# Optimization experiments

Hardware: AMD Instinct MI355X
Metric: run time of the kernel (lower is better)

Reference implementation:

```python
import jax, jax.numpy as jnp
import numpy as np

B, D, K = 32, 64, 26      # batch, n_objects, per-object feature dim
QST = 256                  # question embedding size
G = [512, 512, 512, 512, 512, 512, 28]  # g_layers (last = n_answers)
IN = 2 * K                 # in_size = concat(x_i, x_j)
AGG = 4                    # aggregation + question injection position


def setup_inputs() -> dict:
    key = jax.random.key(0)
    ks = jax.random.split(key, 2 + 2 * len(G))
    inp = {
        "x": jax.random.normal(ks[0], (B, D, K), jnp.float32),
        "qst": jax.random.normal(ks[1], (B, QST), jnp.float32),
    }
    prev = IN
    for i, g in enumerate(G):
        d_in = prev + (QST if i == AGG else 0)
        inp[f"W{i}"] = jax.random.normal(ks[2 + 2 * i], (g, d_in), jnp.float32) * (1.0 / np.sqrt(d_in))
        inp[f"b{i}"] = jnp.zeros((g,), jnp.float32)
        prev = g
    return inp


def reference(x, qst, W0, b0, W1, b1, W2, b2, W3, b3, W4, b4, W5, b5, W6, b6):
    b, d, k = x.shape
    # all ordered pairs: x_full[b, p, q] = [x[b, q], x[b, p]]  (matches torch repeat/cat order)
    xi = jnp.broadcast_to(x[:, None, :, :], (b, d, d, k))
    xj = jnp.broadcast_to(x[:, :, None, :], (b, d, d, k))
    h = jnp.concatenate([xi, xj], axis=-1).reshape(b * d * d, 2 * k)
    Ws = [W0, W1, W2, W3, W4, W5, W6]
    bs = [b0, b1, b2, b3, b4, b5, b6]
    n = len(Ws)
    for i in range(n):
        if i == AGG:
            # sum-aggregation over all d^2 pairs, then question injection
            h = h.reshape(b, d * d, h.shape[-1]).sum(axis=1)  # [b, g]
            h = jnp.concatenate([h, qst], axis=1)             # [b, g+qst]
        h = h @ Ws[i].T + bs[i]
        if i != n - 1:
            h = jax.nn.relu(h)
    return jax.nn.log_softmax(h, axis=1)
```

## Files before the change

kernel.cpp:

```cpp
#include <hip/hip_runtime.h>
#include <math.h>


typedef __attribute__((ext_vector_type(8))) short bf16x8;
typedef __attribute__((ext_vector_type(4))) float f32x4;
typedef __attribute__((ext_vector_type(4))) unsigned int u32x4;

__device__ __forceinline__ unsigned short f2bf(float f) {
    union { float f; unsigned u; } x; x.f = f;
    unsigned r = x.u + 0x7fffu + ((x.u >> 16) & 1u);
    return (unsigned short)(r >> 16);
}

#define NP_WP   786432
#define NP_W0P  32768
#define NP_W4T  393216
#define NP_W5T  262144
#define NP_S    16384
#define NP_TOTAL (NP_WP + NP_W0P + NP_W4T + NP_W5T + NP_S)
__global__ void k_prep(const float* __restrict__ W1, const float* __restrict__ W2,
                       const float* __restrict__ W3, const float* __restrict__ W0,
                       const float* __restrict__ W4, const float* __restrict__ W5,
                       unsigned short* __restrict__ Wp,
                       unsigned short* __restrict__ W0p,
                       float* __restrict__ W4v,
                       float* __restrict__ W5v,
                       float* __restrict__ S)
{
    int f = blockIdx.x * 256 + threadIdx.x;
    if (f < NP_WP) {
        int l = f >> 18, r = f & 262143;
        int n = r >> 9, k = r & 511;
        const float* W = (l == 0) ? W1 : (l == 1) ? W2 : W3;
        float v = W[r];
        int wv = n >> 6, jj = (n >> 4) & 3, i16 = n & 15;
        int s = k >> 5, q4 = (k >> 3) & 3, j = k & 7;
        int lane = q4 * 16 + i16;
        Wp[(size_t)l * 262144 + ((((wv * 16 + s) * 4 + jj) * 64 + lane) << 3) + j] = f2bf(v);
    } else if (f < NP_WP + NP_W0P) {
        int g = f - NP_WP;
        int n = g >> 6, k = g & 63;
        float v = (k < 52) ? W0[n * 52 + k] : 0.f;
        int wv = n >> 6, jj = (n >> 4) & 3, i16 = n & 15;
        int s = k >> 5, q4 = (k >> 3) & 3, j = k & 7;
        int lane = q4 * 16 + i16;
        W0p[((((wv * 2 + s) * 4 + jj) * 64 + lane) << 3) + j] = f2bf(v);
    } else if (f < NP_WP + NP_W0P + NP_W4T) {
        int g = f - (NP_WP + NP_W0P);
        int o = g / 768, k = g % 768;
        W4v[(size_t)((k >> 2) * 512 + o) * 4 + (k & 3)] = W4[g];
    } else if (f < NP_WP + NP_W0P + NP_W4T + NP_W5T) {
        int g = f - (NP_WP + NP_W0P + NP_W4T);
        int o = g >> 9, k = g & 511;
        W5v[(size_t)((k >> 2) * 512 + o) * 4 + (k & 3)] = W5[g];
    } else if (f < NP_TOTAL) {
        S[f - (NP_WP + NP_W0P + NP_W4T + NP_W5T)] = 0.f;
    }
}

__device__ __forceinline__ void store_h(const f32x4 (&acc)[4][4], const float* __restrict__ bl,
                                        unsigned short* hsm, int wave, int i16, int q4, int lane)
{
    char* base = (char*)hsm;
    #pragma unroll
    for (int j = 0; j < 4; ++j) {
        int col = (wave * 4 + j) * 16 + i16;
        int g = col >> 3;
        int e = g & 7;
        float bb = bl[col];
        #pragma unroll
        for (int mt = 0; mt < 4; ++mt) {
            #pragma unroll
            for (int r = 0; r < 4; ++r) {
                int row = mt * 16 + q4 * 4 + r;
                float v = fmaxf(acc[mt][j][r] + bb, 0.f);
                unsigned hv = f2bf(v);
                unsigned sw = (unsigned)__builtin_amdgcn_update_dpp(0, (int)hv, 0xB1, 0xF, 0xF, true);
                if ((lane & 1) == 0) {
                    int slot = row ^ e;
                    *(unsigned*)(base + g * 1024 + slot * 16 + ((col & 7) << 1)) = hv | (sw << 16);
                }
            }
        }
    }
}

__global__ __launch_bounds__(512, 4) void k_fused(
    const float* __restrict__ x,
    const unsigned short* __restrict__ Wp,
    const unsigned short* __restrict__ W0p,
    const float* __restrict__ b0, const float* __restrict__ b1,
    const float* __restrict__ b2, const float* __restrict__ b3,
    float* __restrict__ S)
{
    __shared__ __align__(16) unsigned short hsm[64 * 512];
    __shared__ __align__(16) unsigned short xs[8 * 64 * 8];
    int t = threadIdx.x;
    int blk = blockIdx.x;
    int b = blk >> 6, p = blk & 63;

    {
        int row = t >> 3, gr = t & 7;
        const float* xq = x + (size_t)(b * 64 + row) * 26;
        const float* xp = x + (size_t)(b * 64 + p) * 26;
        unsigned w[4];
        #pragma unroll
        for (int h = 0; h < 4; ++h) {
            int k0 = gr * 8 + h * 2;
            int k1 = k0 + 1;
            float f0 = (k0 < 26) ? xq[k0] : (k0 < 52 ? xp[k0 - 26] : 0.f);
            float f1 = (k1 < 26) ? xq[k1] : (k1 < 52 ? xp[k1 - 26] : 0.f);
            w[h] = (unsigned)f2bf(f0) | ((unsigned)f2bf(f1) << 16);
        }
        *(u32x4*)((char*)xs + gr * 1024 + ((row ^ gr) << 4)) = (u32x4){w[0], w[1], w[2], w[3]};
    }

    int wave = t >> 6, lane = t & 63;
    int i16 = lane & 15, q4 = lane >> 4;

    f32x4 acc[4][4];

    __syncthreads();

    {
        #pragma unroll
        for (int mt = 0; mt < 4; ++mt)
            #pragma unroll
            for (int j = 0; j < 4; ++j)
                acc[mt][j] = (f32x4){0.f, 0.f, 0.f, 0.f};
        const unsigned short* Bb0 = W0p + wave * 4096 + lane * 8;
        const char* xb = (const char*)xs;
        #pragma unroll
        for (int s = 0; s < 2; ++s) {
            bf16x8 bfr[4];
            #pragma unroll
            for (int j = 0; j < 4; ++j)
                bfr[j] = *(const bf16x8*)(Bb0 + s * 2048 + j * 512);
            int g = s * 4 + q4;
            const char* A0 = xb + g * 1024 + ((i16 ^ g) << 4);
            #pragma unroll
            for (int mt = 0; mt < 4; ++mt) {
                bf16x8 a = *(const bf16x8*)(A0 + mt * 256);
                #pragma unroll
                for (int j = 0; j < 4; ++j)
                    acc[mt][j] = __builtin_amdgcn_mfma_f32_16x16x32_bf16(a, bfr[j], acc[mt][j], 0, 0, 0);
            }
        }
        store_h(acc, b0, hsm, wave, i16, q4, lane);
    }

    int A_even = (q4 << 10) + ((i16 ^ q4) << 4);
    int A_odd  = A_even ^ 64;
    const char* hb = (const char*)hsm;

    #pragma unroll 1
    for (int l = 0; l < 3; ++l) {
        const float* bl = (l == 0) ? b1 : (l == 1) ? b2 : b3;
        __syncthreads();

        #pragma unroll
        for (int mt = 0; mt < 4; ++mt)
            #pragma unroll
            for (int j = 0; j < 4; ++j)
                acc[mt][j] = (f32x4){0.f, 0.f, 0.f, 0.f};

        const unsigned short* Bb = Wp + (size_t)l * 262144 + wave * 32768 + lane * 8;

        #pragma unroll 1
        for (int s = 0; s < 16; ++s) {
            bf16x8 bfr[4];
            #pragma unroll
            for (int j = 0; j < 4; ++j)
                bfr[j] = *(const bf16x8*)(Bb + s * 2048 + j * 512);
            const char* Ab = hb + (s << 12) + ((s & 1) ? A_odd : A_even);
            bf16x8 a0 = *(const bf16x8*)(Ab);
            bf16x8 a1 = *(const bf16x8*)(Ab + 256);
            __builtin_amdgcn_s_setprio(1);
            #pragma unroll
            for (int j = 0; j < 4; ++j)
                acc[0][j] = __builtin_amdgcn_mfma_f32_16x16x32_bf16(a0, bfr[j], acc[0][j], 0, 0, 0);
            #pragma unroll
            for (int j = 0; j < 4; ++j)
                acc[1][j] = __builtin_amdgcn_mfma_f32_16x16x32_bf16(a1, bfr[j], acc[1][j], 0, 0, 0);
            __builtin_amdgcn_s_setprio(0);
            bf16x8 a2 = *(const bf16x8*)(Ab + 512);
            bf16x8 a3 = *(const bf16x8*)(Ab + 768);
            __builtin_amdgcn_s_setprio(1);
            #pragma unroll
            for (int j = 0; j < 4; ++j)
                acc[2][j] = __builtin_amdgcn_mfma_f32_16x16x32_bf16(a2, bfr[j], acc[2][j], 0, 0, 0);
            #pragma unroll
            for (int j = 0; j < 4; ++j)
                acc[3][j] = __builtin_amdgcn_mfma_f32_16x16x32_bf16(a3, bfr[j], acc[3][j], 0, 0, 0);
            __builtin_amdgcn_s_setprio(0);
        }
        __syncthreads();

        if (l < 2) {
            store_h(acc, bl, hsm, wave, i16, q4, lane);
        } else {
            #pragma unroll
            for (int j = 0; j < 4; ++j) {
                int col = (wave * 4 + j) * 16 + i16;
                float bb = bl[col];
                float sum = 0.f;
                #pragma unroll
                for (int mt = 0; mt < 4; ++mt)
                    #pragma unroll
                    for (int r = 0; r < 4; ++r)
                        sum += fmaxf(acc[mt][j][r] + bb, 0.f);
                sum += __shfl_xor(sum, 16);
                sum += __shfl_xor(sum, 32);
                if (q4 == 0) atomicAdd(&S[b * 512 + col], sum);
            }
        }
    }
}

__global__ __launch_bounds__(512) void k_tail(
    const float* __restrict__ S, const float* __restrict__ qst,
    const float* __restrict__ W4v, const float* __restrict__ b4,
    const float* __restrict__ W5v, const float* __restrict__ b5,
    const float* __restrict__ W6, const float* __restrict__ b6,
    float* __restrict__ out)
{
    int b = blockIdx.x, t = threadIdx.x;
    __shared__ __align__(16) float z[768];
    __shared__ __align__(16) float h4[512];
    __shared__ float h5[512];
    __shared__ float logits[28];
    __shared__ float red[2];

    for (int i = t; i < 768; i += 512)
        z[i] = (i < 512) ? S[b * 512 + i] : qst[b * 256 + (i - 512)];
    __syncthreads();
    {
        float acc = b4[t];
        const float4* Wv = (const float4*)W4v;
        const float4* z4 = (const float4*)z;
        #pragma unroll 4
        for (int kb = 0; kb < 192; ++kb) {
            float4 w = Wv[kb * 512 + t];
            float4 zz = z4[kb];
            acc = fmaf(w.x, zz.x, acc);
            acc = fmaf(w.y, zz.y, acc);
            acc = fmaf(w.z, zz.z, acc);
            acc = fmaf(w.w, zz.w, acc);
        }
        h4[t] = fmaxf(acc, 0.f);
    }
    __syncthreads();
    {
        float acc = b5[t];
        const float4* Wv = (const float4*)W5v;
        const float4* h44 = (const float4*)h4;
        #pragma unroll 4
        for (int kb = 0; kb < 128; ++kb) {
            float4 w = Wv[kb * 512 + t];
            float4 hh = h44[kb];
            acc = fmaf(w.x, hh.x, acc);
            acc = fmaf(w.y, hh.y, acc);
            acc = fmaf(w.z, hh.z, acc);
            acc = fmaf(w.w, hh.w, acc);
        }
        h5[t] = fmaxf(acc, 0.f);
    }
    __syncthreads();
    {
        int o = t >> 4, c = t & 15;
        if (o < 28) {
            float acc = 0.f;
            for (int k = c; k < 512; k += 16) acc = fmaf(W6[o * 512 + k], h5[k], acc);
            acc += __shfl_xor(acc, 1);
            acc += __shfl_xor(acc, 2);
            acc += __shfl_xor(acc, 4);
            acc += __shfl_xor(acc, 8);
            if (c == 0) logits[o] = acc + b6[o];
        }
    }
    __syncthreads();
    if (t == 0) {
        float mx = -1e30f;
        for (int cc = 0; cc < 28; ++cc) mx = fmaxf(mx, logits[cc]);
        float se = 0.f;
        for (int cc = 0; cc < 28; ++cc) se += expf(logits[cc] - mx);
        red[0] = mx; red[1] = logf(se);
    }
    __syncthreads();
    if (t < 28) out[b * 28 + t] = logits[t] - red[0] - red[1];
}

extern "C" void kernel_launch(void* const* d_in, const int* in_sizes, int n_in,
                              void* d_out, int out_size, void* d_ws, size_t ws_size,
                              hipStream_t stream)
{
    const float* x   = (const float*)d_in[0];
    const float* qst = (const float*)d_in[1];
    const float* W0  = (const float*)d_in[2];
    const float* b0  = (const float*)d_in[3];
    const float* W1  = (const float*)d_in[4];
    const float* b1  = (const float*)d_in[5];
    const float* W2  = (const float*)d_in[6];
    const float* b2  = (const float*)d_in[7];
    const float* W3  = (const float*)d_in[8];
    const float* b3  = (const float*)d_in[9];
    const float* W4  = (const float*)d_in[10];
    const float* b4  = (const float*)d_in[11];
    const float* W5  = (const float*)d_in[12];
    const float* b5  = (const float*)d_in[13];
    const float* W6  = (const float*)d_in[14];
    const float* b6  = (const float*)d_in[15];
    float* out = (float*)d_out;

    char* ws = (char*)d_ws;
    unsigned short* Wp  = (unsigned short*)(ws);
    unsigned short* W0p = (unsigned short*)(ws + 1572864);
    float*          W4v = (float*)(ws + 1638400);
    float*          W5v = (float*)(ws + 3211264);
    float*          S   = (float*)(ws + 4259840);

    k_prep <<<NP_TOTAL / 256, 256, 0, stream>>>(W1, W2, W3, W0, W4, W5,
                                                Wp, W0p, W4v, W5v, S);
    k_fused<<<2048, 512, 0, stream>>>(x, Wp, W0p, b0, b1, b2, b3, S);
    k_tail <<<32, 512, 0, stream>>>(S, qst, W4v, b4, W5v, b5, W6, b6, out);
}
```

Measured before the change: 370.3 us.

## Double-buffer weight fragments, replace atomics with partial buffer, widen tail kernel

The inner GEMM loop is unrolled by two and prefetches the next k-step's B fragments from global memory while the current step's MFMAs run, hiding load latency. The atomic accumulation into S is replaced by per-block partial sums written to a buffer and reduced in the tail kernel. That also removes the zero-init of S from the prep kernel. The tail kernel now uses 1024 threads and splits the K dimension of layers 4 and 5 into two halves, at the cost of extra registers in the fused kernel and a 4 MB partial buffer read in the tail.

```diff
diff --git a/kernel.cpp b/kernel.cpp
--- a/kernel.cpp
+++ b/kernel.cpp
@@ -16,16 +16,14 @@
 #define NP_W0P  32768
 #define NP_W4T  393216
 #define NP_W5T  262144
-#define NP_S    16384
-#define NP_TOTAL (NP_WP + NP_W0P + NP_W4T + NP_W5T + NP_S)
+#define NP_TOTAL (NP_WP + NP_W0P + NP_W4T + NP_W5T)
 __global__ void k_prep(const float* __restrict__ W1, const float* __restrict__ W2,
                        const float* __restrict__ W3, const float* __restrict__ W0,
                        const float* __restrict__ W4, const float* __restrict__ W5,
                        unsigned short* __restrict__ Wp,
                        unsigned short* __restrict__ W0p,
                        float* __restrict__ W4v,
-                       float* __restrict__ W5v,
-                       float* __restrict__ S)
+                       float* __restrict__ W5v)
 {
     int f = blockIdx.x * 256 + threadIdx.x;
     if (f < NP_WP) {
@@ -49,12 +47,10 @@
         int g = f - (NP_WP + NP_W0P);
         int o = g / 768, k = g % 768;
         W4v[(size_t)((k >> 2) * 512 + o) * 4 + (k & 3)] = W4[g];
-    } else if (f < NP_WP + NP_W0P + NP_W4T + NP_W5T) {
+    } else {
         int g = f - (NP_WP + NP_W0P + NP_W4T);
         int o = g >> 9, k = g & 511;
         W5v[(size_t)((k >> 2) * 512 + o) * 4 + (k & 3)] = W5[g];
-    } else if (f < NP_TOTAL) {
-        S[f - (NP_WP + NP_W0P + NP_W4T + NP_W5T)] = 0.f;
     }
 }
 
@@ -91,7 +87,7 @@
     const unsigned short* __restrict__ W0p,
     const float* __restrict__ b0, const float* __restrict__ b1,
     const float* __restrict__ b2, const float* __restrict__ b3,
-    float* __restrict__ S)
+    float* __restrict__ P)
 {
     __shared__ __align__(16) unsigned short hsm[64 * 512];
     __shared__ __align__(16) unsigned short xs[8 * 64 * 8];
@@ -156,6 +152,12 @@
     #pragma unroll 1
     for (int l = 0; l < 3; ++l) {
         const float* bl = (l == 0) ? b1 : (l == 1) ? b2 : b3;
+        const unsigned short* Bb = Wp + (size_t)l * 262144 + wave * 32768 + lane * 8;
+
+        bf16x8 bfr[4], bfrN[4];
+        #pragma unroll
+        for (int j = 0; j < 4; ++j) bfr[j] = *(const bf16x8*)(Bb + j * 512);
+
         __syncthreads();
 
         #pragma unroll
@@ -164,35 +166,61 @@
             for (int j = 0; j < 4; ++j)
                 acc[mt][j] = (f32x4){0.f, 0.f, 0.f, 0.f};
 
-        const unsigned short* Bb = Wp + (size_t)l * 262144 + wave * 32768 + lane * 8;
-
         #pragma unroll 1
-        for (int s = 0; s < 16; ++s) {
-            bf16x8 bfr[4];
-            #pragma unroll
-            for (int j = 0; j < 4; ++j)
-                bfr[j] = *(const bf16x8*)(Bb + s * 2048 + j * 512);
-            const char* Ab = hb + (s << 12) + ((s & 1) ? A_odd : A_even);
-            bf16x8 a0 = *(const bf16x8*)(Ab);
-            bf16x8 a1 = *(const bf16x8*)(Ab + 256);
-            __builtin_amdgcn_s_setprio(1);
-            #pragma unroll
-            for (int j = 0; j < 4; ++j)
-                acc[0][j] = __builtin_amdgcn_mfma_f32_16x16x32_bf16(a0, bfr[j], acc[0][j], 0, 0, 0);
-            #pragma unroll
-            for (int j = 0; j < 4; ++j)
-                acc[1][j] = __builtin_amdgcn_mfma_f32_16x16x32_bf16(a1, bfr[j], acc[1][j], 0, 0, 0);
-            __builtin_amdgcn_s_setprio(0);
-            bf16x8 a2 = *(const bf16x8*)(Ab + 512);
-            bf16x8 a3 = *(const bf16x8*)(Ab + 768);
-            __builtin_amdgcn_s_setprio(1);
-            #pragma unroll
-            for (int j = 0; j < 4; ++j)
-                acc[2][j] = __builtin_amdgcn_mfma_f32_16x16x32_bf16(a2, bfr[j], acc[2][j], 0, 0, 0);
-            #pragma unroll
-            for (int j = 0; j < 4; ++j)
-                acc[3][j] = __builtin_amdgcn_mfma_f32_16x16x32_bf16(a3, bfr[j], acc[3][j], 0, 0, 0);
-            __builtin_amdgcn_s_setprio(0);
+        for (int s = 0; s < 16; s += 2) {
+            {
+                #pragma unroll
+                for (int j = 0; j < 4; ++j)
+                    bfrN[j] = *(const bf16x8*)(Bb + (s + 1) * 2048 + j * 512);
+                const char* Ab = hb + (s << 12) + A_even;
+                bf16x8 a0 = *(const bf16x8*)(Ab);
+                bf16x8 a1 = *(const bf16x8*)(Ab + 256);
+                __builtin_amdgcn_s_setprio(1);
+                #pragma unroll
+                for (int j = 0; j < 4; ++j)
+                    acc[0][j] = __builtin_amdgcn_mfma_f32_16x16x32_bf16(a0, bfr[j], acc[0][j], 0, 0, 0);
+                #pragma unroll
+                for (int j = 0; j < 4; ++j)
+                    acc[1][j] = __builtin_amdgcn_mfma_f32_16x16x32_bf16(a1, bfr[j], acc[1][j], 0, 0, 0);
+                __builtin_amdgcn_s_setprio(0);
+                bf16x8 a2 = *(const bf16x8*)(Ab + 512);
+                bf16x8 a3 = *(const bf16x8*)(Ab + 768);
+                __builtin_amdgcn_s_setprio(1);
+                #pragma unroll
+                for (int j = 0; j < 4; ++j)
+                    acc[2][j] = __builtin_amdgcn_mfma_f32_16x16x32_bf16(a2, bfr[j], acc[2][j], 0, 0, 0);
+                #pragma unroll
+                for (int j = 0; j < 4; ++j)
+                    acc[3][j] = __builtin_amdgcn_mfma_f32_16x16x32_bf16(a3, bfr[j], acc[3][j], 0, 0, 0);
+                __builtin_amdgcn_s_setprio(0);
+            }
+            {
+                int s2 = (s + 2 < 16) ? (s + 2) : 14;
+                #pragma unroll
+                for (int j = 0; j < 4; ++j)
+                    bfr[j] = *(const bf16x8*)(Bb + s2 * 2048 + j * 512);
+                const char* Ab = hb + ((s + 1) << 12) + A_odd;
+                bf16x8 a0 = *(const bf16x8*)(Ab);
+                bf16x8 a1 = *(const bf16x8*)(Ab + 256);
+                __builtin_amdgcn_s_setprio(1);
+                #pragma unroll
+                for (int j = 0; j < 4; ++j)
+                    acc[0][j] = __builtin_amdgcn_mfma_f32_16x16x32_bf16(a0, bfrN[j], acc[0][j], 0, 0, 0);
+                #pragma unroll
+                for (int j = 0; j < 4; ++j)
+                    acc[1][j] = __builtin_amdgcn_mfma_f32_16x16x32_bf16(a1, bfrN[j], acc[1][j], 0, 0, 0);
+                __builtin_amdgcn_s_setprio(0);
+                bf16x8 a2 = *(const bf16x8*)(Ab + 512);
+                bf16x8 a3 = *(const bf16x8*)(Ab + 768);
+                __builtin_amdgcn_s_setprio(1);
+                #pragma unroll
+                for (int j = 0; j < 4; ++j)
+                    acc[2][j] = __builtin_amdgcn_mfma_f32_16x16x32_bf16(a2, bfrN[j], acc[2][j], 0, 0, 0);
+                #pragma unroll
+                for (int j = 0; j < 4; ++j)
+                    acc[3][j] = __builtin_amdgcn_mfma_f32_16x16x32_bf16(a3, bfrN[j], acc[3][j], 0, 0, 0);
+                __builtin_amdgcn_s_setprio(0);
+            }
         }
         __syncthreads();
 
@@ -211,14 +239,14 @@
                         sum += fmaxf(acc[mt][j][r] + bb, 0.f);
                 sum += __shfl_xor(sum, 16);
                 sum += __shfl_xor(sum, 32);
-                if (q4 == 0) atomicAdd(&S[b * 512 + col], sum);
-            }
-        }
-    }
-}
-
-__global__ __launch_bounds__(512) void k_tail(
-    const float* __restrict__ S, const float* __restrict__ qst,
+                if (q4 == 0) P[(size_t)blk * 512 + col] = sum;
+            }
+        }
+    }
+}
+
+__global__ __launch_bounds__(1024) void k_tail(
+    const float* __restrict__ P, const float* __restrict__ qst,
     const float* __restrict__ W4v, const float* __restrict__ b4,
     const float* __restrict__ W5v, const float* __restrict__ b5,
     const float* __restrict__ W6, const float* __restrict__ b6,
@@ -226,55 +254,70 @@
 {
     int b = blockIdx.x, t = threadIdx.x;
     __shared__ __align__(16) float z[768];
+    __shared__ __align__(16) float ps[1024];
     __shared__ __align__(16) float h4[512];
     __shared__ float h5[512];
     __shared__ float logits[28];
     __shared__ float red[2];
 
-    for (int i = t; i < 768; i += 512)
-        z[i] = (i < 512) ? S[b * 512 + i] : qst[b * 256 + (i - 512)];
-    __syncthreads();
-    {
-        float acc = b4[t];
+    if (t < 512) {
+        float s = 0.f;
+        const float* Pb = P + (size_t)b * 64 * 512 + t;
+        #pragma unroll 8
+        for (int c = 0; c < 64; ++c) s += Pb[c * 512];
+        z[t] = s;
+    } else if (t < 768) {
+        z[t] = qst[b * 256 + (t - 512)];
+    }
+    __syncthreads();
+    {
+        int o = t & 511, hf = t >> 9;
+        float acc = 0.f;
         const float4* Wv = (const float4*)W4v;
         const float4* z4 = (const float4*)z;
         #pragma unroll 4
-        for (int kb = 0; kb < 192; ++kb) {
-            float4 w = Wv[kb * 512 + t];
+        for (int kb = hf * 96; kb < hf * 96 + 96; ++kb) {
+            float4 w = Wv[kb * 512 + o];
             float4 zz = z4[kb];
             acc = fmaf(w.x, zz.x, acc);
             acc = fmaf(w.y, zz.y, acc);
             acc = fmaf(w.z, zz.z, acc);
             acc = fmaf(w.w, zz.w, acc);
         }
-        h4[t] = fmaxf(acc, 0.f);
-    }
-    __syncthreads();
-    {
-        float acc = b5[t];
+        ps[t] = acc;
+    }
+    __syncthreads();
+    if (t < 512) h4[t] = fmaxf(ps[t] + ps[t + 512] + b4[t], 0.f);
+    __syncthreads();
+    {
+        int o = t & 511, hf = t >> 9;
+        float acc = 0.f;
         const float4* Wv = (const float4*)W5v;
         const float4* h44 = (const float4*)h4;
         #pragma unroll 4
-        for (int kb = 0; kb < 128; ++kb) {
-            float4 w = Wv[kb * 512 + t];
+        for (int kb = hf * 64; kb < hf * 64 + 64; ++kb) {
+            float4 w = Wv[kb * 512 + o];
             float4 hh = h44[kb];
             acc = fmaf(w.x, hh.x, acc);
             acc = fmaf(w.y, hh.y, acc);
             acc = fmaf(w.z, hh.z, acc);
             acc = fmaf(w.w, hh.w, acc);
         }
-        h5[t] = fmaxf(acc, 0.f);
-    }
-    __syncthreads();
-    {
-        int o = t >> 4, c = t & 15;
+        ps[t] = acc;
+    }
+    __syncthreads();
+    if (t < 512) h5[t] = fmaxf(ps[t] + ps[t + 512] + b5[t], 0.f);
+    __syncthreads();
+    {
+        int o = t >> 5, c = t & 31;
         if (o < 28) {
             float acc = 0.f;
-            for (int k = c; k < 512; k += 16) acc = fmaf(W6[o * 512 + k], h5[k], acc);
+            for (int k = c; k < 512; k += 32) acc = fmaf(W6[o * 512 + k], h5[k], acc);
             acc += __shfl_xor(acc, 1);
             acc += __shfl_xor(acc, 2);
             acc += __shfl_xor(acc, 4);
             acc += __shfl_xor(acc, 8);
+            acc += __shfl_xor(acc, 16);
             if (c == 0) logits[o] = acc + b6[o];
         }
     }
@@ -317,10 +360,10 @@
     unsigned short* W0p = (unsigned short*)(ws + 1572864);
     float*          W4v = (float*)(ws + 1638400);
     float*          W5v = (float*)(ws + 3211264);
-    float*          S   = (float*)(ws + 4259840);
+    float*          P   = (float*)(ws + 4259840);
 
     k_prep <<<NP_TOTAL / 256, 256, 0, stream>>>(W1, W2, W3, W0, W4, W5,
-                                                Wp, W0p, W4v, W5v, S);
-    k_fused<<<2048, 512, 0, stream>>>(x, Wp, W0p, b0, b1, b2, b3, S);
-    k_tail <<<32, 512, 0, stream>>>(S, qst, W4v, b4, W5v, b5, W6, b6, out);
-}
+                                                Wp, W0p, W4v, W5v);
+    k_fused<<<2048, 512, 0, stream>>>(x, Wp, W0p, b0, b1, b2, b3, P);
+    k_tail <<<32, 1024, 0, stream>>>(P, qst, W4v, b4, W5v, b5, W6, b6, out);
+}
```

Result: slower. 413.7 us (+11.7%).
